# Optimization experiments

Hardware: AMD Instinct MI355X
Metric: run time of the kernel (lower is better)

## Reference

```python
import jax, jax.numpy as jnp
import numpy as np

WIN = 7
K1, K2 = 0.01, 0.03


def _box_filter(x, w):
    """Valid-padding uniform box filter. x: (B, D, H, W); w: (1, 1, k, k)."""
    B, D, H, Wd = x.shape
    k = w.shape[-1]
    y = jax.lax.conv_general_dilated(
        x.reshape(B * D, 1, H, Wd), w, window_strides=(1, 1), padding='VALID',
        dimension_numbers=('NCHW', 'OIHW', 'NCHW'))
    return y.reshape(B, D, H - k + 1, Wd - k + 1)


def setup_inputs() -> dict:
    key = jax.random.key(0)
    kx, ky = jax.random.split(key)
    X = jax.random.uniform(kx, (4, 64, 256, 256), dtype=jnp.float32)
    Y = jax.random.uniform(ky, (4, 64, 256, 256), dtype=jnp.float32)
    w = jnp.ones((1, 1, WIN, WIN), dtype=jnp.float32) / (WIN * WIN)  # buffer self.w
    return {"X": X, "Y": Y, "w": w}


def reference(X, Y, w):
    data_range = 1.0
    C1 = (K1 * data_range) ** 2
    C2 = (K2 * data_range) ** 2
    NP = WIN * WIN
    cov_norm = NP / (NP - 1)

    ux = _box_filter(X, w)
    uy = _box_filter(Y, w)
    uxx = _box_filter(X * X, w)
    uyy = _box_filter(Y * Y, w)
    uxy = _box_filter(X * Y, w)

    vx = cov_norm * (uxx - ux * ux)
    vy = cov_norm * (uyy - uy * uy)
    vxy = cov_norm * (uxy - ux * uy)

    A1 = 2.0 * ux * uy + C1
    A2 = 2.0 * vxy + C2
    B1 = ux * ux + uy * uy + C1
    B2 = vx + vy + C2
    S = (A1 * A2) / (B1 * B2)  # (B, D, H', W')

    # Faithful to torch: ssim_per_slice[:, i] = S_i.mean() (mean over batch AND spatial),
    # then 1 - mean over depth, returned per batch element.
    slice_means = S.mean(axis=(0, 2, 3))  # (D,)
    loss = 1.0 - slice_means.mean()
    return jnp.full((X.shape[0],), loss, dtype=X.dtype)
```

## Files before the change

### kernel.cpp

```cpp
#include <hip/hip_runtime.h>

#define H 256
#define W 256
#define W4 (W / 4)
#define OWID 250
#define OHEI 250
#define NIMG 256
#define BAND 14
#define NBANDS 18
#define NBLK (NBANDS * NIMG)

__device__ __forceinline__ float4 f4zero() { return make_float4(0.f, 0.f, 0.f, 0.f); }

__device__ __forceinline__ void vacc(float4& s, const float4 n, const float4 o) {
    s.x += n.x - o.x; s.y += n.y - o.y; s.z += n.z - o.z; s.w += n.w - o.w;
}
__device__ __forceinline__ void vaccp(float4& s, const float4 a, const float4 b,
                                      const float4 c, const float4 d) {
    s.x += a.x * b.x - c.x * d.x;
    s.y += a.y * b.y - c.y * d.y;
    s.z += a.z * b.z - c.z * d.z;
    s.w += a.w * b.w - c.w * d.w;
}

__global__ __launch_bounds__(64) void ssim_band_kernel(
    const float* __restrict__ X, const float* __restrict__ Y,
    float* __restrict__ partial)
{
    const int lane = threadIdx.x;
    const int band = blockIdx.x;
    const int img  = blockIdx.y;
    const int r0 = band * BAND;
    const int out_rows = (OHEI - r0 < BAND) ? (OHEI - r0) : BAND;
    const int rows_in = out_rows + 6;

    const float4* Xp = (const float4*)X + ((size_t)img * H + r0) * W4 + lane;
    const float4* Yp = (const float4*)Y + ((size_t)img * H + r0) * W4 + lane;

    float4 xh[7], yh[7];
    float4 sx = f4zero(), sy = f4zero(), sxx = f4zero(), syy = f4zero(), sxy = f4zero();

    #pragma unroll
    for (int i = 0; i < 6; ++i) {
        float4 xv = Xp[i * W4];
        float4 yv = Yp[i * W4];
        xh[i] = xv; yh[i] = yv;
        vacc(sx, xv, f4zero());
        vacc(sy, yv, f4zero());
        vaccp(sxx, xv, xv, f4zero(), f4zero());
        vaccp(syy, yv, yv, f4zero(), f4zero());
        vaccp(sxy, xv, yv, f4zero(), f4zero());
    }
    xh[6] = f4zero(); yh[6] = f4zero();

    float4 xn = Xp[6 * W4];
    float4 yn = Yp[6 * W4];

    const float C1  = 1e-4f;
    const float C2  = 9e-4f;
    const float AA  = 1.f / 2401.f;
    const float C2A = 2.f / 2401.f;
    const float T1  = 1.f / 24.f;
    const float T2  = -1.f / 1176.f;
    const float T3  = 1.f / 48.f;
    const float T4  = -1.f / 2352.f;
    float lsum = 0.0f;

    for (int base = 6; base < rows_in; base += 7) {
        #pragma unroll
        for (int i = 0; i < 7; ++i) {
            const int r = base + i;
            if (r < rows_in) {
                const int slot = (6 + i) % 7;
                float4 xf, yf;
                const bool more = (r + 1 < rows_in);
                if (more) { xf = Xp[(r + 1) * W4]; yf = Yp[(r + 1) * W4]; }

                const float4 xo = xh[slot], yo = yh[slot];
                vacc(sx, xn, xo);
                vacc(sy, yn, yo);
                vaccp(sxx, xn, xn, xo, xo);
                vaccp(syy, yn, yn, yo, yo);
                vaccp(sxy, xn, yn, xo, yo);
                xh[slot] = xn; yh[slot] = yn;

                float wx[4], wy[4], wxx[4], wyy[4], wxy[4];
                #define HWIN(S, WA)                                            \
                {                                                              \
                    const float bx = __shfl_down(S.x, 1);                      \
                    const float by = __shfl_down(S.y, 1);                      \
                    const float bz = __shfl_down(S.z, 1);                      \
                    const float bw = __shfl_down(S.w, 1);                      \
                    const float cx = __shfl_down(S.x, 2);                      \
                    const float cy = __shfl_down(S.y, 2);                      \
                    WA[0] = S.x + S.y + S.z + S.w + bx + by + bz;              \
                    WA[1] = WA[0] - S.x + bw;                                  \
                    WA[2] = WA[1] - S.y + cx;                                  \
                    WA[3] = WA[2] - S.z + cy;                                  \
                }
                HWIN(sx,  wx)
                HWIN(sy,  wy)
                HWIN(sxx, wxx)
                HWIN(syy, wyy)
                HWIN(sxy, wxy)
                #undef HWIN

                #pragma unroll
                for (int s = 0; s < 4; ++s) {
                    const float P  = wx[s] * wy[s];
                    const float Qs = fmaf(wy[s], wy[s], wx[s] * wx[s]);
                    const float Ws = wxx[s] + wyy[s];
                    const float A1 = fmaf(C2A, P, C1);
                    const float B1 = fmaf(AA, Qs, C1);
                    const float A2 = fmaf(T1, wxy[s], fmaf(T2, P, C2));
                    const float B2 = fmaf(T3, Ws, fmaf(T4, Qs, C2));
                    const float S  = (A1 * A2) * __builtin_amdgcn_rcpf(B1 * B2);
                    if (4 * lane + s < OWID) lsum += S;
                }
                xn = xf; yn = yf;
            }
        }
    }

    #pragma unroll
    for (int off = 32; off > 0; off >>= 1)
        lsum += __shfl_down(lsum, off, 64);
    if (lane == 0) partial[img * NBANDS + band] = lsum;
}

__global__ __launch_bounds__(256) void ssim_reduce_kernel(
    const float* __restrict__ partial, float* __restrict__ out)
{
    const int tid = threadIdx.x;
    double acc = 0.0;
    for (int i = tid; i < NBLK; i += 256)
        acc += (double)partial[i];
    #pragma unroll
    for (int off = 32; off > 0; off >>= 1)
        acc += __shfl_down(acc, off, 64);
    __shared__ double wsumd[4];
    if ((tid & 63) == 0) wsumd[tid >> 6] = acc;
    __syncthreads();
    if (tid == 0) {
        double total = wsumd[0] + wsumd[1] + wsumd[2] + wsumd[3];
        float loss = (float)(1.0 - total / 16000000.0);
        out[0] = loss; out[1] = loss; out[2] = loss; out[3] = loss;
    }
}

extern "C" void kernel_launch(void* const* d_in, const int* in_sizes, int n_in,
                              void* d_out, int out_size, void* d_ws, size_t ws_size,
                              hipStream_t stream) {
    const float* X = (const float*)d_in[0];
    const float* Y = (const float*)d_in[1];
    float* out = (float*)d_out;
    float* partial = (float*)d_ws;

    hipLaunchKernelGGL(ssim_band_kernel, dim3(NBANDS, NIMG), dim3(64), 0, stream,
                       X, Y, partial);
    hipLaunchKernelGGL(ssim_reduce_kernel, dim3(1), dim3(256), 0, stream,
                       partial, out);
}
```

Baseline: 161.3 us.

## Merge xx+yy sums, fully unroll fixed 10-row bands with double-buffered loads

Folds the separate x² and y² running sums into one x²+y² sum, since the SSIM formula only uses their sum. This drops one accumulator and one horizontal shuffle-window pass per row. Bands shrink to 10 output rows (25 bands) so every block handles exactly 16 input rows, letting the loop fully unroll with compile-time history slots and a two-deep prefetch. Occupancy is hinted via launch bounds. The trade-off is more halo re-reads from the smaller bands, and the merged sum could change float rounding slightly.

```diff
diff --git a/kernel.cpp b/kernel.cpp
--- a/kernel.cpp
+++ b/kernel.cpp
@@ -4,26 +4,15 @@
 #define W 256
 #define W4 (W / 4)
 #define OWID 250
-#define OHEI 250
 #define NIMG 256
-#define BAND 14
-#define NBANDS 18
+#define BAND 10
+#define NBANDS 25
 #define NBLK (NBANDS * NIMG)
+#define RIN 16
 
 __device__ __forceinline__ float4 f4zero() { return make_float4(0.f, 0.f, 0.f, 0.f); }
 
-__device__ __forceinline__ void vacc(float4& s, const float4 n, const float4 o) {
-    s.x += n.x - o.x; s.y += n.y - o.y; s.z += n.z - o.z; s.w += n.w - o.w;
-}
-__device__ __forceinline__ void vaccp(float4& s, const float4 a, const float4 b,
-                                      const float4 c, const float4 d) {
-    s.x += a.x * b.x - c.x * d.x;
-    s.y += a.y * b.y - c.y * d.y;
-    s.z += a.z * b.z - c.z * d.z;
-    s.w += a.w * b.w - c.w * d.w;
-}
-
-__global__ __launch_bounds__(64) void ssim_band_kernel(
+__global__ __launch_bounds__(64, 4) void ssim_band_kernel(
     const float* __restrict__ X, const float* __restrict__ Y,
     float* __restrict__ partial)
 {
@@ -31,30 +20,17 @@
     const int band = blockIdx.x;
     const int img  = blockIdx.y;
     const int r0 = band * BAND;
-    const int out_rows = (OHEI - r0 < BAND) ? (OHEI - r0) : BAND;
-    const int rows_in = out_rows + 6;
 
     const float4* Xp = (const float4*)X + ((size_t)img * H + r0) * W4 + lane;
     const float4* Yp = (const float4*)Y + ((size_t)img * H + r0) * W4 + lane;
 
     float4 xh[7], yh[7];
-    float4 sx = f4zero(), sy = f4zero(), sxx = f4zero(), syy = f4zero(), sxy = f4zero();
+    float4 sx = f4zero(), sy = f4zero(), sxy = f4zero(), spp = f4zero();
 
-    #pragma unroll
-    for (int i = 0; i < 6; ++i) {
-        float4 xv = Xp[i * W4];
-        float4 yv = Yp[i * W4];
-        xh[i] = xv; yh[i] = yv;
-        vacc(sx, xv, f4zero());
-        vacc(sy, yv, f4zero());
-        vaccp(sxx, xv, xv, f4zero(), f4zero());
-        vaccp(syy, yv, yv, f4zero(), f4zero());
-        vaccp(sxy, xv, yv, f4zero(), f4zero());
-    }
-    xh[6] = f4zero(); yh[6] = f4zero();
-
-    float4 xn = Xp[6 * W4];
-    float4 yn = Yp[6 * W4];
+    float4 px[2], py[2];
+    px[0] = Xp[0];      py[0] = Yp[0];
+    px[1] = Xp[W4];     py[1] = Yp[W4];
+    xh[6] = f4zero();   yh[6] = f4zero();
 
     const float C1  = 1e-4f;
     const float C2  = 9e-4f;
@@ -66,58 +42,74 @@
     const float T4  = -1.f / 2352.f;
     float lsum = 0.0f;
 
-    for (int base = 6; base < rows_in; base += 7) {
-        #pragma unroll
-        for (int i = 0; i < 7; ++i) {
-            const int r = base + i;
-            if (r < rows_in) {
-                const int slot = (6 + i) % 7;
-                float4 xf, yf;
-                const bool more = (r + 1 < rows_in);
-                if (more) { xf = Xp[(r + 1) * W4]; yf = Yp[(r + 1) * W4]; }
+    #pragma unroll
+    for (int r = 0; r < RIN; ++r) {
+        const float4 xn = px[r & 1], yn = py[r & 1];
+        if (r + 2 < RIN) {
+            px[r & 1] = Xp[(r + 2) * W4];
+            py[r & 1] = Yp[(r + 2) * W4];
+        }
 
-                const float4 xo = xh[slot], yo = yh[slot];
-                vacc(sx, xn, xo);
-                vacc(sy, yn, yo);
-                vaccp(sxx, xn, xn, xo, xo);
-                vaccp(syy, yn, yn, yo, yo);
-                vaccp(sxy, xn, yn, xo, yo);
-                xh[slot] = xn; yh[slot] = yn;
+        if (r < 6) {
+            xh[r] = xn; yh[r] = yn;
+            sx.x += xn.x; sx.y += xn.y; sx.z += xn.z; sx.w += xn.w;
+            sy.x += yn.x; sy.y += yn.y; sy.z += yn.z; sy.w += yn.w;
+            sxy.x = fmaf(xn.x, yn.x, sxy.x);
+            sxy.y = fmaf(xn.y, yn.y, sxy.y);
+            sxy.z = fmaf(xn.z, yn.z, sxy.z);
+            sxy.w = fmaf(xn.w, yn.w, sxy.w);
+            spp.x = fmaf(xn.x, xn.x, fmaf(yn.x, yn.x, spp.x));
+            spp.y = fmaf(xn.y, xn.y, fmaf(yn.y, yn.y, spp.y));
+            spp.z = fmaf(xn.z, xn.z, fmaf(yn.z, yn.z, spp.z));
+            spp.w = fmaf(xn.w, xn.w, fmaf(yn.w, yn.w, spp.w));
+        } else {
+            const int slot = r % 7;
+            const float4 xo = xh[slot], yo = yh[slot];
 
-                float wx[4], wy[4], wxx[4], wyy[4], wxy[4];
-                #define HWIN(S, WA)                                            \
-                {                                                              \
-                    const float bx = __shfl_down(S.x, 1);                      \
-                    const float by = __shfl_down(S.y, 1);                      \
-                    const float bz = __shfl_down(S.z, 1);                      \
-                    const float bw = __shfl_down(S.w, 1);                      \
-                    const float cx = __shfl_down(S.x, 2);                      \
-                    const float cy = __shfl_down(S.y, 2);                      \
-                    WA[0] = S.x + S.y + S.z + S.w + bx + by + bz;              \
-                    WA[1] = WA[0] - S.x + bw;                                  \
-                    WA[2] = WA[1] - S.y + cx;                                  \
-                    WA[3] = WA[2] - S.z + cy;                                  \
-                }
-                HWIN(sx,  wx)
-                HWIN(sy,  wy)
-                HWIN(sxx, wxx)
-                HWIN(syy, wyy)
-                HWIN(sxy, wxy)
-                #undef HWIN
+            sx.x += xn.x - xo.x; sx.y += xn.y - xo.y;
+            sx.z += xn.z - xo.z; sx.w += xn.w - xo.w;
+            sy.x += yn.x - yo.x; sy.y += yn.y - yo.y;
+            sy.z += yn.z - yo.z; sy.w += yn.w - yo.w;
+            sxy.x = fmaf(xn.x, yn.x, fmaf(-xo.x, yo.x, sxy.x));
+            sxy.y = fmaf(xn.y, yn.y, fmaf(-xo.y, yo.y, sxy.y));
+            sxy.z = fmaf(xn.z, yn.z, fmaf(-xo.z, yo.z, sxy.z));
+            sxy.w = fmaf(xn.w, yn.w, fmaf(-xo.w, yo.w, sxy.w));
+            spp.x = fmaf(xn.x, xn.x, fmaf(yn.x, yn.x, fmaf(-xo.x, xo.x, fmaf(-yo.x, yo.x, spp.x))));
+            spp.y = fmaf(xn.y, xn.y, fmaf(yn.y, yn.y, fmaf(-xo.y, xo.y, fmaf(-yo.y, yo.y, spp.y))));
+            spp.z = fmaf(xn.z, xn.z, fmaf(yn.z, yn.z, fmaf(-xo.z, xo.z, fmaf(-yo.z, yo.z, spp.z))));
+            spp.w = fmaf(xn.w, xn.w, fmaf(yn.w, yn.w, fmaf(-xo.w, xo.w, fmaf(-yo.w, yo.w, spp.w))));
+            xh[slot] = xn; yh[slot] = yn;
 
-                #pragma unroll
-                for (int s = 0; s < 4; ++s) {
-                    const float P  = wx[s] * wy[s];
-                    const float Qs = fmaf(wy[s], wy[s], wx[s] * wx[s]);
-                    const float Ws = wxx[s] + wyy[s];
-                    const float A1 = fmaf(C2A, P, C1);
-                    const float B1 = fmaf(AA, Qs, C1);
-                    const float A2 = fmaf(T1, wxy[s], fmaf(T2, P, C2));
-                    const float B2 = fmaf(T3, Ws, fmaf(T4, Qs, C2));
-                    const float S  = (A1 * A2) * __builtin_amdgcn_rcpf(B1 * B2);
-                    if (4 * lane + s < OWID) lsum += S;
-                }
-                xn = xf; yn = yf;
+            float wx[4], wy[4], wpp[4], wxy[4];
+            #define HWIN(S, WA)                                            \
+            {                                                              \
+                const float bx = __shfl_down(S.x, 1);                      \
+                const float by = __shfl_down(S.y, 1);                      \
+                const float bz = __shfl_down(S.z, 1);                      \
+                const float bw = __shfl_down(S.w, 1);                      \
+                const float cx = __shfl_down(S.x, 2);                      \
+                const float cy = __shfl_down(S.y, 2);                      \
+                WA[0] = S.x + S.y + S.z + S.w + bx + by + bz;              \
+                WA[1] = WA[0] - S.x + bw;                                  \
+                WA[2] = WA[1] - S.y + cx;                                  \
+                WA[3] = WA[2] - S.z + cy;                                  \
+            }
+            HWIN(sx,  wx)
+            HWIN(sy,  wy)
+            HWIN(spp, wpp)
+            HWIN(sxy, wxy)
+            #undef HWIN
+
+            #pragma unroll
+            for (int s = 0; s < 4; ++s) {
+                const float P  = wx[s] * wy[s];
+                const float Qs = fmaf(wy[s], wy[s], wx[s] * wx[s]);
+                const float A1 = fmaf(C2A, P, C1);
+                const float B1 = fmaf(AA, Qs, C1);
+                const float A2 = fmaf(T1, wxy[s], fmaf(T2, P, C2));
+                const float B2 = fmaf(T3, wpp[s], fmaf(T4, Qs, C2));
+                const float S  = (A1 * A2) * __builtin_amdgcn_rcpf(B1 * B2);
+                if (4 * lane + s < OWID) lsum += S;
             }
         }
     }
```

Measured after the change: 156.9 us. 2.7% less time.
